# Performance work log

Measured on AMD Instinct MI355X. Metric: run time of the kernel, lower is better.

## Reference

```python
import jax, jax.numpy as jnp
import numpy as np

N = 1048576  # rays * samples per batch
IN_DIM = 32          # hashgrid encoder output (16 levels x 2 feats)
SH_DIM = 16          # degree-4 spherical harmonics
HID = 64
GEO = 15


def sh_encode(v):
    """Real spherical harmonics up to degree 4 (16 comps), v: [N,3] unit vecs."""
    x, y, z = v[..., 0], v[..., 1], v[..., 2]
    xx, yy, zz = x * x, y * y, z * z
    xy, yz, xz = x * y, y * z, x * z
    comps = [
        jnp.full_like(x, 0.28209479177387814),
        -0.48860251190291987 * y,
        0.48860251190291987 * z,
        -0.48860251190291987 * x,
        1.0925484305920792 * xy,
        -1.0925484305920792 * yz,
        0.94617469575755997 * zz - 0.31539156525252005,
        -1.0925484305920792 * xz,
        0.54627421529603959 * (xx - yy),
        0.59004358992664352 * y * (3.0 * xx - yy),
        2.8906114426405538 * xy * z,
        0.45704579946446572 * y * (4.0 * zz - xx - yy),
        0.3731763325901154 * z * (2.0 * zz - 3.0 * xx - 3.0 * yy),
        0.45704579946446572 * x * (4.0 * zz - xx - yy),
        1.445305721320277 * z * (xx - yy),
        0.5900435899266435 * x * (xx - 3.0 * yy),
    ]
    return jnp.stack(comps, axis=-1)


def _w(key, fan_in, fan_out):
    return jax.random.normal(key, (fan_in, fan_out), dtype=jnp.float32) / np.sqrt(fan_in)


def setup_inputs() -> dict:
    key = jax.random.key(0)
    ks = jax.random.split(key, 12)
    x_feat = jax.random.normal(ks[0], (N, IN_DIM), dtype=jnp.float32)
    d = jax.random.normal(ks[1], (N, 3), dtype=jnp.float32)
    d = d / jnp.linalg.norm(d, axis=-1, keepdims=True)
    lig = jax.random.normal(ks[2], (N, 3), dtype=jnp.float32)
    lig = lig / jnp.linalg.norm(lig, axis=-1, keepdims=True)
    return {
        "x_feat": x_feat, "d": d, "lig": lig,
        # sigma net: 32 -> 64 -> 1+15
        "w_sig0": _w(ks[3], IN_DIM, HID),
        "w_sig1": _w(ks[4], HID, 1 + GEO),
        # color net: (16+16+32) -> 64, (64+15) -> 64, 64 -> 3
        "w_col0": _w(ks[5], SH_DIM + SH_DIM + IN_DIM, HID),
        "w_col1": _w(ks[6], HID + GEO, HID),
        "w_col2": _w(ks[7], HID, 3),
        # vis net (only 2 layers run in forward): (16+32) -> 64, 64 -> 1
        "w_vis0": _w(ks[8], SH_DIM + IN_DIM, HID),
        "w_vis1": _w(ks[9], HID, 1),
    }


def reference(x_feat, d, lig, w_sig0, w_sig1, w_col0, w_col1, w_col2, w_vis0, w_vis1):
    # sigma tower (bias-free)
    h = jax.nn.relu(x_feat @ w_sig0)
    h = h @ w_sig1                      # [N, 1+GEO]
    geo_feat = h[..., 1:]               # sigma = trunc_exp(h[...,0]) is unused in output

    d_enc = sh_encode(d)                # [N,16]
    l_enc = sh_encode(lig)              # [N,16]

    # color tower: cat([h_x, light, d]) then cat geo_feat before layer 1
    hc = jnp.concatenate([x_feat, l_enc, d_enc], axis=-1)
    hc = jax.nn.relu(hc @ w_col0)
    hc = jnp.concatenate([hc, geo_feat], axis=-1)
    hc = jax.nn.relu(hc @ w_col1)
    hc = hc @ w_col2
    color = jax.nn.relu(hc)             # [N,3]

    # vis tower: cat([h_x, light]), 2 layers (range(num_layers))
    hv = jnp.concatenate([x_feat, l_enc], axis=-1)
    hv = jax.nn.relu(hv @ w_vis0)
    hv = hv @ w_vis1
    vis = jax.nn.sigmoid(hv)            # [N,1]

    return color * vis                  # broadcast -> [N,3]
```

## Files before the change

kernel.cpp:

```cpp
#include <hip/hip_runtime.h>
#include <math.h>

#define BLOCK 256
#define GRID  2048

typedef _Float16 half8  __attribute__((ext_vector_type(8)));
typedef __fp16   fp16x2 __attribute__((ext_vector_type(2)));
typedef float    f32x4  __attribute__((ext_vector_type(4)));

__device__ __forceinline__ int phi(int nt, int m) {
    return ((nt >> 1) << 5) + ((m >> 2) << 3) + ((nt & 1) << 2) + (m & 3);
}

__device__ __forceinline__ half8 bfragW(const float* __restrict__ w, int N0,
                                        int nsrc, int k0, int Kreal, bool valid) {
    half8 r;
    #pragma unroll
    for (int j = 0; j < 8; j++) {
        int k = k0 + j;
        float v = (valid && k < Kreal) ? w[k * N0 + nsrc] : 0.f;
        r[j] = (_Float16)v;
    }
    return r;
}

__device__ __forceinline__ half8 packrelu(f32x4 a, f32x4 b) {
    half8 h; fp16x2 p;
    p = __builtin_amdgcn_cvt_pkrtz(fmaxf(a[0], 0.f), fmaxf(a[1], 0.f)); h[0]=p[0]; h[1]=p[1];
    p = __builtin_amdgcn_cvt_pkrtz(fmaxf(a[2], 0.f), fmaxf(a[3], 0.f)); h[2]=p[0]; h[3]=p[1];
    p = __builtin_amdgcn_cvt_pkrtz(fmaxf(b[0], 0.f), fmaxf(b[1], 0.f)); h[4]=p[0]; h[5]=p[1];
    p = __builtin_amdgcn_cvt_pkrtz(fmaxf(b[2], 0.f), fmaxf(b[3], 0.f)); h[6]=p[0]; h[7]=p[1];
    return h;
}

__device__ __forceinline__ half8 packraw(f32x4 a, f32x4 b) {
    half8 h; fp16x2 p;
    p = __builtin_amdgcn_cvt_pkrtz(a[0], a[1]); h[0]=p[0]; h[1]=p[1];
    p = __builtin_amdgcn_cvt_pkrtz(a[2], a[3]); h[2]=p[0]; h[3]=p[1];
    p = __builtin_amdgcn_cvt_pkrtz(b[0], b[1]); h[4]=p[0]; h[5]=p[1];
    p = __builtin_amdgcn_cvt_pkrtz(b[2], b[3]); h[6]=p[0]; h[7]=p[1];
    return h;
}

__device__ __forceinline__ half8 shfrag(float x, float y, float z, bool hi) {
    float xx = x * x, yy = y * y, zz = z * z;
    float xy = x * y, yz = y * z, xz = x * z;
    float e0  = 0.28209479177387814f;
    float e1  = -0.48860251190291987f * y;
    float e2  = 0.48860251190291987f * z;
    float e3  = -0.48860251190291987f * x;
    float e4  = 1.0925484305920792f * xy;
    float e5  = -1.0925484305920792f * yz;
    float e6  = 0.94617469575756f * zz - 0.31539156525252005f;
    float e7  = -1.0925484305920792f * xz;
    float e8  = 0.5462742152960396f * (xx - yy);
    float e9  = 0.5900435899266435f * y * (3.0f * xx - yy);
    float e10 = 2.890611442640554f * xy * z;
    float e11 = 0.4570457994644657f * y * (4.0f * zz - xx - yy);
    float e12 = 0.3731763325901154f * z * (2.0f * zz - 3.0f * xx - 3.0f * yy);
    float e13 = 0.4570457994644657f * x * (4.0f * zz - xx - yy);
    float e14 = 1.445305721320277f * z * (xx - yy);
    float e15 = 0.5900435899266435f * x * (xx - 3.0f * yy);
    float s0 = hi ? e8  : e0, s1 = hi ? e9  : e1;
    float s2 = hi ? e10 : e2, s3 = hi ? e11 : e3;
    float s4 = hi ? e12 : e4, s5 = hi ? e13 : e5;
    float s6 = hi ? e14 : e6, s7 = hi ? e15 : e7;
    half8 r; fp16x2 p;
    p = __builtin_amdgcn_cvt_pkrtz(s0, s1); r[0]=p[0]; r[1]=p[1];
    p = __builtin_amdgcn_cvt_pkrtz(s2, s3); r[2]=p[0]; r[3]=p[1];
    p = __builtin_amdgcn_cvt_pkrtz(s4, s5); r[4]=p[0]; r[5]=p[1];
    p = __builtin_amdgcn_cvt_pkrtz(s6, s7); r[6]=p[0]; r[7]=p[1];
    return r;
}

__device__ __forceinline__ half8 cvt8(float4 v0, float4 v1) {
    half8 f; fp16x2 p;
    p = __builtin_amdgcn_cvt_pkrtz(v0.x, v0.y); f[0]=p[0]; f[1]=p[1];
    p = __builtin_amdgcn_cvt_pkrtz(v0.z, v0.w); f[2]=p[0]; f[3]=p[1];
    p = __builtin_amdgcn_cvt_pkrtz(v1.x, v1.y); f[4]=p[0]; f[5]=p[1];
    p = __builtin_amdgcn_cvt_pkrtz(v1.z, v1.w); f[6]=p[0]; f[7]=p[1];
    return f;
}

#define MFMA(A, B, C) __builtin_amdgcn_mfma_f32_16x16x32_f16((A), (B), (C), 0, 0, 0)
#define SBAR() __builtin_amdgcn_sched_barrier(0)

#define NFRAG  40
#define F_SIG0 0
#define F_COL0 4
#define F_VIS0 12
#define F_SIG1 20
#define F_VIS1 24
#define F_COL1 26
#define F_COL2 38

__global__ __launch_bounds__(BLOCK, 4) void nerf_pk(
    const float* __restrict__ x_feat,
    const float* __restrict__ dvec,
    const float* __restrict__ lvec,
    const float* __restrict__ w_sig0,
    const float* __restrict__ w_sig1,
    const float* __restrict__ w_col0,
    const float* __restrict__ w_col1,
    const float* __restrict__ w_col2,
    const float* __restrict__ w_vis0,
    const float* __restrict__ w_vis1,
    float* __restrict__ out, int n)
{
    const int tid  = threadIdx.x;
    const int wv   = tid >> 6;
    const int lane = tid & 63;
    const int m    = lane & 15;
    const int q    = lane >> 4;

    __shared__ half8 WL[NFRAG * 64];

    const float* dl = (q < 2) ? lvec : dvec;
    const int ntiles = n >> 7;

    float4 rxa0, rxa1, rxb0, rxb1;
    float rvax, rvay, rvaz, rvbx, rvby, rvbz;
    {
        const int t0  = blockIdx.x;
        const int pt0 = (t0 << 7) + wv * 32 + m;
        const int pt1 = pt0 + 16;
        const float4* xa = (const float4*)(x_feat + (size_t)pt0 * 32 + q * 8);
        rxa0 = xa[0]; rxa1 = xa[1];
        const float4* xb = (const float4*)(x_feat + (size_t)pt1 * 32 + q * 8);
        rxb0 = xb[0]; rxb1 = xb[1];
        const float* va = dl + (size_t)pt0 * 3;
        rvax = va[0]; rvay = va[1]; rvaz = va[2];
        const float* vb = dl + (size_t)pt1 * 3;
        rvbx = vb[0]; rvby = vb[1]; rvbz = vb[2];
    }

    if (wv == 0) {
        #pragma unroll
        for (int nt = 0; nt < 4; nt++)
            WL[(F_SIG0 + nt) * 64 + lane] =
                bfragW(w_sig0, 64, phi(nt, m), q * 8, 32, true);
        #pragma unroll
        for (int nt = 0; nt < 2; nt++)
            #pragma unroll
            for (int kt = 0; kt < 2; kt++) {
                int g = ((m >> 2) << 3) + ((nt & 1) << 2) + (m & 3);
                bool valid = ((m >> 2) < 2) && (g < 15);
                WL[(F_SIG1 + nt * 2 + kt) * 64 + lane] =
                    bfragW(w_sig1, 16, g + 1, kt * 32 + q * 8, 64, valid);
            }
        #pragma unroll
        for (int kt = 0; kt < 2; kt++)
            WL[(F_VIS1 + kt) * 64 + lane] =
                bfragW(w_vis1, 1, 0, kt * 32 + q * 8, 64, m == 0);
    } else if (wv == 1) {
        #pragma unroll
        for (int nt = 0; nt < 4; nt++)
            #pragma unroll
            for (int kt = 0; kt < 2; kt++)
                WL[(F_COL0 + nt * 2 + kt) * 64 + lane] =
                    bfragW(w_col0, 64, phi(nt, m), kt * 32 + q * 8, 64, true);
        #pragma unroll
        for (int kt = 0; kt < 2; kt++)
            WL[(F_COL2 + kt) * 64 + lane] =
                bfragW(w_col2, 3, m, kt * 32 + q * 8, 64, m < 3);
    } else if (wv == 2) {
        #pragma unroll
        for (int nt = 0; nt < 4; nt++)
            #pragma unroll
            for (int kt = 0; kt < 2; kt++)
                WL[(F_VIS0 + nt * 2 + kt) * 64 + lane] =
                    bfragW(w_vis0, 64, phi(nt, m), kt * 32 + q * 8, 48, true);
    } else {
        #pragma unroll
        for (int nt = 0; nt < 4; nt++)
            #pragma unroll
            for (int kt = 0; kt < 3; kt++)
                WL[(F_COL1 + nt * 3 + kt) * 64 + lane] =
                    bfragW(w_col1, 64, phi(nt, m), kt * 32 + q * 8, 79, true);
    }
    __syncthreads();

    int wl = lane;
    #define LW(f) WL[wl + (f) * 64]

    const f32x4 z = {0.f, 0.f, 0.f, 0.f};
    for (int t = blockIdx.x; t < ntiles; t += GRID) {
        asm volatile("" : "+v"(wl));

        const int pt0 = (t << 7) + wv * 32 + m;
        const int pt1 = pt0 + 16;

        half8 fA0 = cvt8(rxa0, rxa1);
        half8 fB0 = cvt8(rxb0, rxb1);
        half8 fA1 = shfrag(rvax, rvay, rvaz, (q & 1) != 0);
        half8 fB1 = shfrag(rvbx, rvby, rvbz, (q & 1) != 0);

        {
            int tn = t + GRID;
            int tp = (tn < ntiles) ? tn : t;
            const int qt0 = (tp << 7) + wv * 32 + m;
            const int qt1 = qt0 + 16;
            const float4* xa = (const float4*)(x_feat + (size_t)qt0 * 32 + q * 8);
            rxa0 = xa[0]; rxa1 = xa[1];
            const float4* xb = (const float4*)(x_feat + (size_t)qt1 * 32 + q * 8);
            rxb0 = xb[0]; rxb1 = xb[1];
            const float* va = dl + (size_t)qt0 * 3;
            rvax = va[0]; rvay = va[1]; rvaz = va[2];
            const float* vb = dl + (size_t)qt1 * 3;
            rvbx = vb[0]; rvby = vb[1]; rvbz = vb[2];
        }

        half8 w;
        f32x4 aA, aB, bA, bB;

        w = LW(F_SIG0 + 0); aA = MFMA(w, fA0, z); aB = MFMA(w, fB0, z);
        w = LW(F_SIG0 + 1); bA = MFMA(w, fA0, z); bB = MFMA(w, fB0, z);
        half8 hK0a = packrelu(aA, bA), hK0b = packrelu(aB, bB);
        w = LW(F_SIG0 + 2); aA = MFMA(w, fA0, z); aB = MFMA(w, fB0, z);
        w = LW(F_SIG0 + 3); bA = MFMA(w, fA0, z); bB = MFMA(w, fB0, z);
        half8 hK1a = packrelu(aA, bA), hK1b = packrelu(aB, bB);
        SBAR();

        w = LW(F_SIG1 + 0); aA = MFMA(w, hK0a, z);  aB = MFMA(w, hK0b, z);
        w = LW(F_SIG1 + 1); aA = MFMA(w, hK1a, aA); aB = MFMA(w, hK1b, aB);
        w = LW(F_SIG1 + 2); bA = MFMA(w, hK0a, z);  bB = MFMA(w, hK0b, z);
        w = LW(F_SIG1 + 3); bA = MFMA(w, hK1a, bA); bB = MFMA(w, hK1b, bB);
        half8 gA = packraw(aA, bA), gB = packraw(aB, bB);
        SBAR();

        w = LW(F_COL0 + 0); aA = MFMA(w, fA0, z);  aB = MFMA(w, fB0, z);
        w = LW(F_COL0 + 1); aA = MFMA(w, fA1, aA); aB = MFMA(w, fB1, aB);
        w = LW(F_COL0 + 2); bA = MFMA(w, fA0, z);  bB = MFMA(w, fB0, z);
        w = LW(F_COL0 + 3); bA = MFMA(w, fA1, bA); bB = MFMA(w, fB1, bB);
        half8 cK0a = packrelu(aA, bA), cK0b = packrelu(aB, bB);
        w = LW(F_COL0 + 4); aA = MFMA(w, fA0, z);  aB = MFMA(w, fB0, z);
        w = LW(F_COL0 + 5); aA = MFMA(w, fA1, aA); aB = MFMA(w, fB1, aB);
        w = LW(F_COL0 + 6); bA = MFMA(w, fA0, z);  bB = MFMA(w, fB0, z);
        w = LW(F_COL0 + 7); bA = MFMA(w, fA1, bA); bB = MFMA(w, fB1, bB);
        half8 cK1a = packrelu(aA, bA), cK1b = packrelu(aB, bB);
        SBAR();

        w = LW(F_VIS0 + 0); aA = MFMA(w, fA0, z);  aB = MFMA(w, fB0, z);
        w = LW(F_VIS0 + 1); aA = MFMA(w, fA1, aA); aB = MFMA(w, fB1, aB);
        w = LW(F_VIS0 + 2); bA = MFMA(w, fA0, z);  bB = MFMA(w, fB0, z);
        w = LW(F_VIS0 + 3); bA = MFMA(w, fA1, bA); bB = MFMA(w, fB1, bB);
        half8 vK0a = packrelu(aA, bA), vK0b = packrelu(aB, bB);
        w = LW(F_VIS0 + 4); aA = MFMA(w, fA0, z);  aB = MFMA(w, fB0, z);
        w = LW(F_VIS0 + 5); aA = MFMA(w, fA1, aA); aB = MFMA(w, fB1, aB);
        w = LW(F_VIS0 + 6); bA = MFMA(w, fA0, z);  bB = MFMA(w, fB0, z);
        w = LW(F_VIS0 + 7); bA = MFMA(w, fA1, bA); bB = MFMA(w, fB1, bB);
        half8 vK1a = packrelu(aA, bA), vK1b = packrelu(aB, bB);

        f32x4 va = z, vb = z;
        w = LW(F_VIS1 + 0); va = MFMA(w, vK0a, va); vb = MFMA(w, vK0b, vb);
        w = LW(F_VIS1 + 1); va = MFMA(w, vK1a, va); vb = MFMA(w, vK1b, vb);
        float visA = 1.f / (1.f + __expf(-va[0]));
        float visB = 1.f / (1.f + __expf(-vb[0]));
        SBAR();

        w = LW(F_COL1 + 0);  aA = MFMA(w, cK0a, z);  aB = MFMA(w, cK0b, z);
        w = LW(F_COL1 + 1);  aA = MFMA(w, cK1a, aA); aB = MFMA(w, cK1b, aB);
        w = LW(F_COL1 + 2);  aA = MFMA(w, gA,   aA); aB = MFMA(w, gB,   aB);
        w = LW(F_COL1 + 3);  bA = MFMA(w, cK0a, z);  bB = MFMA(w, cK0b, z);
        w = LW(F_COL1 + 4);  bA = MFMA(w, cK1a, bA); bB = MFMA(w, cK1b, bB);
        w = LW(F_COL1 + 5);  bA = MFMA(w, gA,   bA); bB = MFMA(w, gB,   bB);
        half8 h2K0a = packrelu(aA, bA), h2K0b = packrelu(aB, bB);
        w = LW(F_COL1 + 6);  aA = MFMA(w, cK0a, z);  aB = MFMA(w, cK0b, z);
        w = LW(F_COL1 + 7);  aA = MFMA(w, cK1a, aA); aB = MFMA(w, cK1b, aB);
        w = LW(F_COL1 + 8);  aA = MFMA(w, gA,   aA); aB = MFMA(w, gB,   aB);
        w = LW(F_COL1 + 9);  bA = MFMA(w, cK0a, z);  bB = MFMA(w, cK0b, z);
        w = LW(F_COL1 + 10); bA = MFMA(w, cK1a, bA); bB = MFMA(w, cK1b, bB);
        w = LW(F_COL1 + 11); bA = MFMA(w, gA,   bA); bB = MFMA(w, gB,   bB);
        half8 h2K1a = packrelu(aA, bA), h2K1b = packrelu(aB, bB);
        SBAR();

        f32x4 ca = z, cb = z;
        w = LW(F_COL2 + 0); ca = MFMA(w, h2K0a, ca); cb = MFMA(w, h2K0b, cb);
        w = LW(F_COL2 + 1); ca = MFMA(w, h2K1a, ca); cb = MFMA(w, h2K1b, cb);
        if (q == 0) {
            float* oa = out + (size_t)pt0 * 3;
            oa[0] = fmaxf(ca[0], 0.f) * visA;
            oa[1] = fmaxf(ca[1], 0.f) * visA;
            oa[2] = fmaxf(ca[2], 0.f) * visA;
            float* ob = out + (size_t)pt1 * 3;
            ob[0] = fmaxf(cb[0], 0.f) * visB;
            ob[1] = fmaxf(cb[1], 0.f) * visB;
            ob[2] = fmaxf(cb[2], 0.f) * visB;
        }
    }
    #undef LW
}

extern "C" void kernel_launch(void* const* d_in, const int* in_sizes, int n_in,
                              void* d_out, int out_size, void* d_ws, size_t ws_size,
                              hipStream_t stream) {
    const float* x_feat = (const float*)d_in[0];
    const float* dvec   = (const float*)d_in[1];
    const float* lvec   = (const float*)d_in[2];
    const float* w_sig0 = (const float*)d_in[3];
    const float* w_sig1 = (const float*)d_in[4];
    const float* w_col0 = (const float*)d_in[5];
    const float* w_col1 = (const float*)d_in[6];
    const float* w_col2 = (const float*)d_in[7];
    const float* w_vis0 = (const float*)d_in[8];
    const float* w_vis1 = (const float*)d_in[9];
    float* out = (float*)d_out;

    const int n = in_sizes[0] / 32;
    nerf_pk<<<GRID, BLOCK, 0, stream>>>(x_feat, dvec, lvec,
                                        w_sig0, w_sig1, w_col0, w_col1,
                                        w_col2, w_vis0, w_vis1, out, n);
}
```

Baseline: 243.8 us.

## Split SH encoding across lane pairs with ds_swizzle and pack ReLU in fp16

Each lane now loads one direction vector and computes all 16 SH components for one point, not half the components for two points. The halves are exchanged between quad groups with ds_swizzle, which removes duplicated SH arithmetic and a second vector load per lane. ReLU is moved after fp16 packing and done as a packed half max, and the occupancy hint in launch_bounds drops from 4 to 3. The swizzle pattern must pair lanes correctly, and the lower occupancy hint may reduce latency hiding.

```diff
diff --git a/kernel.cpp b/kernel.cpp
--- a/kernel.cpp
+++ b/kernel.cpp
@@ -7,6 +7,7 @@
 typedef _Float16 half8  __attribute__((ext_vector_type(8)));
 typedef __fp16   fp16x2 __attribute__((ext_vector_type(2)));
 typedef float    f32x4  __attribute__((ext_vector_type(4)));
+typedef unsigned int uint4v __attribute__((ext_vector_type(4)));
 
 __device__ __forceinline__ int phi(int nt, int m) {
     return ((nt >> 1) << 5) + ((m >> 2) << 3) + ((nt & 1) << 2) + (m & 3);
@@ -24,62 +25,37 @@
     return r;
 }
 
+__device__ __forceinline__ unsigned pk2u(float a, float b) {
+    return __builtin_bit_cast(unsigned, __builtin_amdgcn_cvt_pkrtz(a, b));
+}
+
+__device__ __forceinline__ half8 mk8(unsigned a, unsigned b, unsigned c, unsigned d) {
+    uint4v t; t[0] = a; t[1] = b; t[2] = c; t[3] = d;
+    return __builtin_bit_cast(half8, t);
+}
+
 __device__ __forceinline__ half8 packrelu(f32x4 a, f32x4 b) {
-    half8 h; fp16x2 p;
-    p = __builtin_amdgcn_cvt_pkrtz(fmaxf(a[0], 0.f), fmaxf(a[1], 0.f)); h[0]=p[0]; h[1]=p[1];
-    p = __builtin_amdgcn_cvt_pkrtz(fmaxf(a[2], 0.f), fmaxf(a[3], 0.f)); h[2]=p[0]; h[3]=p[1];
-    p = __builtin_amdgcn_cvt_pkrtz(fmaxf(b[0], 0.f), fmaxf(b[1], 0.f)); h[4]=p[0]; h[5]=p[1];
-    p = __builtin_amdgcn_cvt_pkrtz(fmaxf(b[2], 0.f), fmaxf(b[3], 0.f)); h[6]=p[0]; h[7]=p[1];
-    return h;
+    half8 h = mk8(pk2u(a[0], a[1]), pk2u(a[2], a[3]),
+                  pk2u(b[0], b[1]), pk2u(b[2], b[3]));
+#if __has_builtin(__builtin_elementwise_max)
+    const half8 hz = {0, 0, 0, 0, 0, 0, 0, 0};
+    return __builtin_elementwise_max(h, hz);
+#else
+    half8 r;
+    #pragma unroll
+    for (int i = 0; i < 8; i++) r[i] = h[i] > (_Float16)0 ? h[i] : (_Float16)0;
+    return r;
+#endif
 }
 
 __device__ __forceinline__ half8 packraw(f32x4 a, f32x4 b) {
-    half8 h; fp16x2 p;
-    p = __builtin_amdgcn_cvt_pkrtz(a[0], a[1]); h[0]=p[0]; h[1]=p[1];
-    p = __builtin_amdgcn_cvt_pkrtz(a[2], a[3]); h[2]=p[0]; h[3]=p[1];
-    p = __builtin_amdgcn_cvt_pkrtz(b[0], b[1]); h[4]=p[0]; h[5]=p[1];
-    p = __builtin_amdgcn_cvt_pkrtz(b[2], b[3]); h[6]=p[0]; h[7]=p[1];
-    return h;
-}
-
-__device__ __forceinline__ half8 shfrag(float x, float y, float z, bool hi) {
-    float xx = x * x, yy = y * y, zz = z * z;
-    float xy = x * y, yz = y * z, xz = x * z;
-    float e0  = 0.28209479177387814f;
-    float e1  = -0.48860251190291987f * y;
-    float e2  = 0.48860251190291987f * z;
-    float e3  = -0.48860251190291987f * x;
-    float e4  = 1.0925484305920792f * xy;
-    float e5  = -1.0925484305920792f * yz;
-    float e6  = 0.94617469575756f * zz - 0.31539156525252005f;
-    float e7  = -1.0925484305920792f * xz;
-    float e8  = 0.5462742152960396f * (xx - yy);
-    float e9  = 0.5900435899266435f * y * (3.0f * xx - yy);
-    float e10 = 2.890611442640554f * xy * z;
-    float e11 = 0.4570457994644657f * y * (4.0f * zz - xx - yy);
-    float e12 = 0.3731763325901154f * z * (2.0f * zz - 3.0f * xx - 3.0f * yy);
-    float e13 = 0.4570457994644657f * x * (4.0f * zz - xx - yy);
-    float e14 = 1.445305721320277f * z * (xx - yy);
-    float e15 = 0.5900435899266435f * x * (xx - 3.0f * yy);
-    float s0 = hi ? e8  : e0, s1 = hi ? e9  : e1;
-    float s2 = hi ? e10 : e2, s3 = hi ? e11 : e3;
-    float s4 = hi ? e12 : e4, s5 = hi ? e13 : e5;
-    float s6 = hi ? e14 : e6, s7 = hi ? e15 : e7;
-    half8 r; fp16x2 p;
-    p = __builtin_amdgcn_cvt_pkrtz(s0, s1); r[0]=p[0]; r[1]=p[1];
-    p = __builtin_amdgcn_cvt_pkrtz(s2, s3); r[2]=p[0]; r[3]=p[1];
-    p = __builtin_amdgcn_cvt_pkrtz(s4, s5); r[4]=p[0]; r[5]=p[1];
-    p = __builtin_amdgcn_cvt_pkrtz(s6, s7); r[6]=p[0]; r[7]=p[1];
-    return r;
+    return mk8(pk2u(a[0], a[1]), pk2u(a[2], a[3]),
+               pk2u(b[0], b[1]), pk2u(b[2], b[3]));
 }
 
 __device__ __forceinline__ half8 cvt8(float4 v0, float4 v1) {
-    half8 f; fp16x2 p;
-    p = __builtin_amdgcn_cvt_pkrtz(v0.x, v0.y); f[0]=p[0]; f[1]=p[1];
-    p = __builtin_amdgcn_cvt_pkrtz(v0.z, v0.w); f[2]=p[0]; f[3]=p[1];
-    p = __builtin_amdgcn_cvt_pkrtz(v1.x, v1.y); f[4]=p[0]; f[5]=p[1];
-    p = __builtin_amdgcn_cvt_pkrtz(v1.z, v1.w); f[6]=p[0]; f[7]=p[1];
-    return f;
+    return mk8(pk2u(v0.x, v0.y), pk2u(v0.z, v0.w),
+               pk2u(v1.x, v1.y), pk2u(v1.z, v1.w));
 }
 
 #define MFMA(A, B, C) __builtin_amdgcn_mfma_f32_16x16x32_f16((A), (B), (C), 0, 0, 0)
@@ -94,7 +70,7 @@
 #define F_COL1 26
 #define F_COL2 38
 
-__global__ __launch_bounds__(BLOCK, 4) void nerf_pk(
+__global__ __launch_bounds__(BLOCK, 3) void nerf_sw(
     const float* __restrict__ x_feat,
     const float* __restrict__ dvec,
     const float* __restrict__ lvec,
@@ -112,6 +88,7 @@
     const int lane = tid & 63;
     const int m    = lane & 15;
     const int q    = lane >> 4;
+    const bool odd = (q & 1) != 0;
 
     __shared__ half8 WL[NFRAG * 64];
 
@@ -119,7 +96,7 @@
     const int ntiles = n >> 7;
 
     float4 rxa0, rxa1, rxb0, rxb1;
-    float rvax, rvay, rvaz, rvbx, rvby, rvbz;
+    float rvx, rvy, rvz;
     {
         const int t0  = blockIdx.x;
         const int pt0 = (t0 << 7) + wv * 32 + m;
@@ -128,10 +105,8 @@
         rxa0 = xa[0]; rxa1 = xa[1];
         const float4* xb = (const float4*)(x_feat + (size_t)pt1 * 32 + q * 8);
         rxb0 = xb[0]; rxb1 = xb[1];
-        const float* va = dl + (size_t)pt0 * 3;
-        rvax = va[0]; rvay = va[1]; rvaz = va[2];
-        const float* vb = dl + (size_t)pt1 * 3;
-        rvbx = vb[0]; rvby = vb[1]; rvbz = vb[2];
+        const float* vv = dl + (size_t)(odd ? pt1 : pt0) * 3;
+        rvx = vv[0]; rvy = vv[1]; rvz = vv[2];
     }
 
     if (wv == 0) {
@@ -192,8 +167,41 @@
 
         half8 fA0 = cvt8(rxa0, rxa1);
         half8 fB0 = cvt8(rxb0, rxb1);
-        half8 fA1 = shfrag(rvax, rvay, rvaz, (q & 1) != 0);
-        half8 fB1 = shfrag(rvbx, rvby, rvbz, (q & 1) != 0);
+
+        half8 fA1, fB1;
+        {
+            float sx = rvx, sy = rvy, sz = rvz;
+            float xx = sx * sx, yy = sy * sy, zz = sz * sz;
+            float xy = sx * sy, yz = sy * sz, xz = sx * sz;
+            float e0  = 0.28209479177387814f;
+            float e1  = -0.48860251190291987f * sy;
+            float e2  = 0.48860251190291987f * sz;
+            float e3  = -0.48860251190291987f * sx;
+            float e4  = 1.0925484305920792f * xy;
+            float e5  = -1.0925484305920792f * yz;
+            float e6  = 0.94617469575756f * zz - 0.31539156525252005f;
+            float e7  = -1.0925484305920792f * xz;
+            float e8  = 0.5462742152960396f * (xx - yy);
+            float e9  = 0.5900435899266435f * sy * (3.0f * xx - yy);
+            float e10 = 2.890611442640554f * xy * sz;
+            float e11 = 0.4570457994644657f * sy * (4.0f * zz - xx - yy);
+            float e12 = 0.3731763325901154f * sz * (2.0f * zz - 3.0f * xx - 3.0f * yy);
+            float e13 = 0.4570457994644657f * sx * (4.0f * zz - xx - yy);
+            float e14 = 1.445305721320277f * sz * (xx - yy);
+            float e15 = 0.5900435899266435f * sx * (xx - 3.0f * yy);
+            unsigned L0 = pk2u(e0, e1),   L1 = pk2u(e2, e3);
+            unsigned L2 = pk2u(e4, e5),   L3 = pk2u(e6, e7);
+            unsigned H0 = pk2u(e8, e9),   H1 = pk2u(e10, e11);
+            unsigned H2 = pk2u(e12, e13), H3 = pk2u(e14, e15);
+            unsigned S0 = odd ? L0 : H0, S1 = odd ? L1 : H1;
+            unsigned S2 = odd ? L2 : H2, S3 = odd ? L3 : H3;
+            unsigned R0 = (unsigned)__builtin_amdgcn_ds_swizzle((int)S0, 0x401F);
+            unsigned R1 = (unsigned)__builtin_amdgcn_ds_swizzle((int)S1, 0x401F);
+            unsigned R2 = (unsigned)__builtin_amdgcn_ds_swizzle((int)S2, 0x401F);
+            unsigned R3 = (unsigned)__builtin_amdgcn_ds_swizzle((int)S3, 0x401F);
+            fA1 = mk8(odd ? R0 : L0, odd ? R1 : L1, odd ? R2 : L2, odd ? R3 : L3);
+            fB1 = mk8(odd ? H0 : R0, odd ? H1 : R1, odd ? H2 : R2, odd ? H3 : R3);
+        }
 
         {
             int tn = t + GRID;
@@ -204,10 +212,8 @@
             rxa0 = xa[0]; rxa1 = xa[1];
             const float4* xb = (const float4*)(x_feat + (size_t)qt1 * 32 + q * 8);
             rxb0 = xb[0]; rxb1 = xb[1];
-            const float* va = dl + (size_t)qt0 * 3;
-            rvax = va[0]; rvay = va[1]; rvaz = va[2];
-            const float* vb = dl + (size_t)qt1 * 3;
-            rvbx = vb[0]; rvby = vb[1]; rvbz = vb[2];
+            const float* vv = dl + (size_t)(odd ? qt1 : qt0) * 3;
+            rvx = vv[0]; rvy = vv[1]; rvz = vv[2];
         }
 
         half8 w;
@@ -307,7 +313,7 @@
     float* out = (float*)d_out;
 
     const int n = in_sizes[0] / 32;
-    nerf_pk<<<GRID, BLOCK, 0, stream>>>(x_feat, dvec, lvec,
+    nerf_sw<<<GRID, BLOCK, 0, stream>>>(x_feat, dvec, lvec,
                                         w_sig0, w_sig1, w_col0, w_col1,
                                         w_col2, w_vis0, w_vis1, out, n);
 }
```

Result: no change. 241.0 us (-1.1%).
